# Optimization experiments

Hardware: AMD Instinct MI355X
Metric: run time of the kernel (lower is better)

Reference implementation:

```python
import jax, jax.numpy as jnp
import numpy as np

B, K, D, N_SENSES = 512, 32, 768, 200000
NEG_INF = -1e30


def setup_inputs() -> dict:
    key = jax.random.key(0)
    k1, k2, k3 = jax.random.split(key, 3)
    reps = jax.random.normal(k1, (B, D), dtype=jnp.float32)
    weight = jax.random.normal(k2, (N_SENSES, D), dtype=jnp.float32) * 0.02
    bias = jax.random.normal(k3, (N_SENSES,), dtype=jnp.float32) * 0.02
    # Ragged candidate sets: each sample has a variable number of candidate
    # senses in [2, K], remainder padded with -1 (as in the torch code).
    rng = np.random.default_rng(0)
    lengths = rng.integers(2, K + 1, size=B)
    ids = rng.integers(0, N_SENSES, size=(B, K)).astype(np.int64)
    pos = np.arange(K)[None, :]
    ids = np.where(pos < lengths[:, None], ids, -1)
    targets = (rng.integers(0, 1 << 30, size=B) % lengths).astype(np.int64)
    return {
        "reps": reps,
        "weight": weight,
        "bias": bias,
        "sense_ids": jnp.asarray(ids),
        "target_ids": jnp.asarray(targets),
    }


def reference(reps, weight, bias, sense_ids, target_ids):
    # mask of valid (non -1) candidates, [B, K]
    mask = sense_ids >= 0
    ids = jnp.where(mask, sense_ids, 0)
    # ragged gather of candidate rows: [B, K, D] and [B, K]
    w = weight[ids]
    b = bias[ids]
    # per-sample small matvec + bias -> logits [B, K]
    logits = jnp.einsum("bkd,bd->bk", w, reps) + b
    logits = jnp.where(mask, logits, NEG_INF)
    # cross-entropy per sample, summed then divided by B (== mean)
    logp = jax.nn.log_softmax(logits, axis=-1)
    nll = -jnp.take_along_axis(logp, target_ids[:, None], axis=-1)[:, 0]
    loss = jnp.mean(nll)
    correct = jnp.argmax(logits, axis=-1) == target_ids
    return loss, correct
```

## Files before the change

### kernel.cpp

```cpp
#include <hip/hip_runtime.h>
#include <math.h>

#define BB 512
#define KK 32
#define DD 768
#define NEG_INF (-1e30f)

__global__ __launch_bounds__(256) void cbert_logits_kernel(
    const float* __restrict__ reps,
    const float* __restrict__ weight,
    const float* __restrict__ bias,
    const int*   __restrict__ sense_ids,
    const int*   __restrict__ target_ids,
    float* __restrict__ out,
    float* __restrict__ nll_ws)
{
    __shared__ float4 s_repv[DD / 4];
    __shared__ float  s_logits[KK];

    const int b   = blockIdx.x;
    const int tid = threadIdx.x;

    const float4* repv = reinterpret_cast<const float4*>(reps + (size_t)b * DD);
    for (int i = tid; i < DD / 4; i += 256) s_repv[i] = repv[i];
    __syncthreads();

    const int wave = tid >> 6;
    const int lane = tid & 63;

    for (int k = wave; k < KK; k += 4) {
        const int id = sense_ids[b * KK + k];
        float logit;
        if (id < 0) {
            logit = NEG_INF;
        } else {
            const float4* wrow =
                reinterpret_cast<const float4*>(weight + (size_t)id * DD);
            float acc = 0.0f;
            #pragma unroll
            for (int j = 0; j < 3; ++j) {
                const float4 w4 = wrow[j * 64 + lane];
                const float4 r4 = s_repv[j * 64 + lane];
                acc += w4.x * r4.x + w4.y * r4.y + w4.z * r4.z + w4.w * r4.w;
            }
            #pragma unroll
            for (int off = 32; off >= 1; off >>= 1)
                acc += __shfl_down(acc, off, 64);
            logit = acc + bias[id];
        }
        if (lane == 0) s_logits[k] = logit;
    }
    __syncthreads();

    if (tid == 0) {
        float m = s_logits[0];
        int   am = 0;
        for (int k = 1; k < KK; ++k) {
            const float v = s_logits[k];
            if (v > m) { m = v; am = k; }
        }
        float se = 0.0f;
        for (int k = 0; k < KK; ++k) se += expf(s_logits[k] - m);
        const int tgt = target_ids[b];
        const float nll = -(s_logits[tgt] - m - logf(se));
        nll_ws[b]    = nll;
        out[1 + b]   = (am == tgt) ? 1.0f : 0.0f;
    }
}

__global__ __launch_bounds__(64) void cbert_loss_kernel(
    const float* __restrict__ nll_ws, float* __restrict__ out)
{
    const int lane = threadIdx.x;
    float acc = 0.0f;
    for (int i = lane; i < BB; i += 64) acc += nll_ws[i];
    #pragma unroll
    for (int off = 32; off >= 1; off >>= 1)
        acc += __shfl_down(acc, off, 64);
    if (lane == 0) out[0] = acc / (float)BB;
}

extern "C" void kernel_launch(void* const* d_in, const int* in_sizes, int n_in,
                              void* d_out, int out_size, void* d_ws, size_t ws_size,
                              hipStream_t stream) {
    const float* reps       = (const float*)d_in[0];
    const float* weight     = (const float*)d_in[1];
    const float* bias       = (const float*)d_in[2];
    const int*   sense_ids  = (const int*)d_in[3];
    const int*   target_ids = (const int*)d_in[4];
    float* out    = (float*)d_out;
    float* nll_ws = (float*)d_ws;

    cbert_logits_kernel<<<BB, 256, 0, stream>>>(
        reps, weight, bias, sense_ids, target_ids, out, nll_ws);
    cbert_loss_kernel<<<1, 64, 0, stream>>>(nll_ws, out);
}
```

Before: 668.5 us.

## Widen logits kernel to 1024 threads and issue all row gathers up front

```diff
diff --git a/kernel.cpp b/kernel.cpp
--- a/kernel.cpp
+++ b/kernel.cpp
@@ -6,7 +6,7 @@
 #define DD 768
 #define NEG_INF (-1e30f)
 
-__global__ __launch_bounds__(256) void cbert_logits_kernel(
+__global__ __launch_bounds__(1024) void cbert_logits_kernel(
     const float* __restrict__ reps,
     const float* __restrict__ weight,
     const float* __restrict__ bias,
@@ -22,33 +22,54 @@
     const int tid = threadIdx.x;
 
     const float4* repv = reinterpret_cast<const float4*>(reps + (size_t)b * DD);
-    for (int i = tid; i < DD / 4; i += 256) s_repv[i] = repv[i];
-    __syncthreads();
+    if (tid < DD / 4) s_repv[tid] = repv[tid];
 
     const int wave = tid >> 6;
     const int lane = tid & 63;
+    const int k0 = wave;
+    const int k1 = wave + 16;
 
-    for (int k = wave; k < KK; k += 4) {
-        const int id = sense_ids[b * KK + k];
-        float logit;
-        if (id < 0) {
-            logit = NEG_INF;
-        } else {
-            const float4* wrow =
-                reinterpret_cast<const float4*>(weight + (size_t)id * DD);
-            float acc = 0.0f;
-            #pragma unroll
-            for (int j = 0; j < 3; ++j) {
-                const float4 w4 = wrow[j * 64 + lane];
-                const float4 r4 = s_repv[j * 64 + lane];
-                acc += w4.x * r4.x + w4.y * r4.y + w4.z * r4.z + w4.w * r4.w;
-            }
-            #pragma unroll
-            for (int off = 32; off >= 1; off >>= 1)
-                acc += __shfl_down(acc, off, 64);
-            logit = acc + bias[id];
-        }
-        if (lane == 0) s_logits[k] = logit;
+    const int id0 = sense_ids[b * KK + k0];
+    const int id1 = sense_ids[b * KK + k1];
+    const int g0  = (id0 < 0) ? 0 : id0;
+    const int g1  = (id1 < 0) ? 0 : id1;
+
+    const float4* w0 = reinterpret_cast<const float4*>(weight + (size_t)g0 * DD);
+    const float4* w1 = reinterpret_cast<const float4*>(weight + (size_t)g1 * DD);
+
+    const float4 a0 = w0[0 * 64 + lane];
+    const float4 a1 = w0[1 * 64 + lane];
+    const float4 a2 = w0[2 * 64 + lane];
+    const float4 c0 = w1[0 * 64 + lane];
+    const float4 c1 = w1[1 * 64 + lane];
+    const float4 c2 = w1[2 * 64 + lane];
+    const float bias0 = bias[g0];
+    const float bias1 = bias[g1];
+
+    __syncthreads();
+
+    const float4 r0 = s_repv[0 * 64 + lane];
+    const float4 r1 = s_repv[1 * 64 + lane];
+    const float4 r2 = s_repv[2 * 64 + lane];
+
+    float acc0 = 0.0f;
+    acc0 += a0.x * r0.x + a0.y * r0.y + a0.z * r0.z + a0.w * r0.w;
+    acc0 += a1.x * r1.x + a1.y * r1.y + a1.z * r1.z + a1.w * r1.w;
+    acc0 += a2.x * r2.x + a2.y * r2.y + a2.z * r2.z + a2.w * r2.w;
+    float acc1 = 0.0f;
+    acc1 += c0.x * r0.x + c0.y * r0.y + c0.z * r0.z + c0.w * r0.w;
+    acc1 += c1.x * r1.x + c1.y * r1.y + c1.z * r1.z + c1.w * r1.w;
+    acc1 += c2.x * r2.x + c2.y * r2.y + c2.z * r2.z + c2.w * r2.w;
+
+    #pragma unroll
+    for (int off = 32; off >= 1; off >>= 1) {
+        acc0 += __shfl_down(acc0, off, 64);
+        acc1 += __shfl_down(acc1, off, 64);
+    }
+
+    if (lane == 0) {
+        s_logits[k0] = (id0 < 0) ? NEG_INF : acc0 + bias0;
+        s_logits[k1] = (id1 < 0) ? NEG_INF : acc1 + bias1;
     }
     __syncthreads();
 
@@ -91,7 +112,7 @@
     float* out    = (float*)d_out;
     float* nll_ws = (float*)d_ws;
 
-    cbert_logits_kernel<<<BB, 256, 0, stream>>>(
+    cbert_logits_kernel<<<BB, 1024, 0, stream>>>(
         reps, weight, bias, sense_ids, target_ids, out, nll_ws);
     cbert_loss_kernel<<<1, 64, 0, stream>>>(nll_ws, out);
 }
```

Result: no change. 662.2 us (-0.9%).
